# Optimization experiments

Measured on AMD Instinct MI355X. Metric: run time of the kernel, lower is better.

Reference implementation:

```python
import jax, jax.numpy as jnp
import numpy as np

B, L, D, H = 256, 200, 256, 16
Dh = D // H  # value_dim = 16


def setup_inputs() -> dict:
    key = jax.random.key(0)
    ks = jax.random.split(key, 11)
    s = 0.02
    return {
        "news_repr": jax.random.normal(ks[0], (B, L, D), jnp.float32),
        "his_mask": jax.random.randint(ks[1], (B, L, 1), 0, 2, jnp.int32),
        "Wq": jax.random.normal(ks[2], (D, D), jnp.float32) * s,
        "bq": jnp.zeros((D,), jnp.float32),
        "Wk": jax.random.normal(ks[3], (D, D), jnp.float32) * s,
        "bk": jnp.zeros((D,), jnp.float32),
        "Wv": jax.random.normal(ks[4], (D, D), jnp.float32) * s,
        "bv": jnp.zeros((D,), jnp.float32),
        "Wo": jax.random.normal(ks[5], (D, D), jnp.float32) * s,
        "bo": jnp.zeros((D,), jnp.float32),
        "query_news": jax.random.normal(ks[6], (1, D), jnp.float32),
    }


def reference(news_repr, his_mask, Wq, bq, Wk, bk, Wv, bv, Wo, bo, query_news):
    mask = his_mask[..., 0]                                   # [B, L] int
    # get_attn_mask: additive mask, (1 - m) * -10000, broadcast [B,1,1,L]
    add_mask = (1.0 - mask.astype(jnp.float32)) * -10000.0    # [B, L]

    # hand-rolled multi-head attention over the history
    q = (news_repr @ Wq + bq).reshape(B, L, H, Dh)
    k = (news_repr @ Wk + bk).reshape(B, L, H, Dh)
    v = (news_repr @ Wv + bv).reshape(B, L, H, Dh)
    scores = jnp.einsum('bqhd,bkhd->bhqk', q, k) / np.sqrt(Dh)  # [B,H,L,L]
    scores = scores + add_mask[:, None, None, :]
    attn = jax.nn.softmax(scores, axis=-1)
    ctx = jnp.einsum('bhqk,bkhd->bqhd', attn, v).reshape(B, L, D)
    news_out = ctx @ Wo + bo                                   # [B, L, D]

    # scaled_dp_attention pooling against learned query [1, D]
    ps = jnp.einsum('qd,bld->bql', query_news, news_out) / np.sqrt(D)  # [B,1,L]
    ps = jnp.where(mask[:, None, :] > 0, ps, -1e9)
    pattn = jax.nn.softmax(ps, axis=-1)
    user_repr = jnp.einsum('bql,bld->bqd', pattn, news_out)    # [B,1,D]
    return user_repr
```

## Files before the change

kernel.cpp:

```cpp
#include <hip/hip_runtime.h>

typedef unsigned short u16;
typedef unsigned int u32;
typedef unsigned long long u64;
typedef __attribute__((ext_vector_type(8))) short bfrag;
typedef __attribute__((ext_vector_type(4))) short sfrag;
typedef __attribute__((ext_vector_type(4))) float ffrag;


__device__ __forceinline__ float bf2f(u16 u) {
    union { float f; u32 i; } c; c.i = ((u32)u) << 16; return c.f;
}
__device__ __forceinline__ u16 f2bf(float f) {
    union { float f; u32 i; } c; c.f = f;
    u32 r = c.i + 0x7FFFu + ((c.i >> 16) & 1u);
    return (u16)(r >> 16);
}
__device__ __forceinline__ u32 pack2bf(float lo, float hi) {
    union { float f; u32 i; } a, b; a.f = lo; b.f = hi;
    u32 ra = a.i + 0x7FFFu + ((a.i >> 16) & 1u);
    u32 rb = b.i + 0x7FFFu + ((b.i >> 16) & 1u);
    return (ra >> 16) | (rb & 0xFFFF0000u);
}
__device__ __forceinline__ ffrag mfma16(bfrag a, bfrag b, ffrag c) {
    return __builtin_amdgcn_mfma_f32_16x16x32_bf16(a, b, c, 0, 0, 0);
}
__device__ __forceinline__ ffrag mfma16k16(sfrag a, sfrag b, ffrag c) {
    return __builtin_amdgcn_mfma_f32_16x16x16bf16_1k(a, b, c, 0, 0, 0);
}

__global__ __launch_bounds__(256) void wtrans_k(
    const float* __restrict__ W0, const float* __restrict__ W1,
    const float* __restrict__ W2, const float* __restrict__ W3,
    u16* __restrict__ Wt)
{
    __shared__ u16 t_s[64][72];
    const int mat = blockIdx.z;
    const float* W = (mat == 0) ? W0 : (mat == 1) ? W1 : (mat == 2) ? W2 : W3;
    const int k0 = blockIdx.x * 64, n0 = blockIdx.y * 64;
    const int r = threadIdx.x >> 2, cq = threadIdx.x & 3;

    const float* src = W + (size_t)(k0 + r) * 256 + n0 + cq * 16;
#pragma unroll
    for (int j = 0; j < 16; j += 4) {
        float4 f = *(const float4*)(src + j);
        t_s[cq * 16 + j + 0][r] = f2bf(f.x);
        t_s[cq * 16 + j + 1][r] = f2bf(f.y);
        t_s[cq * 16 + j + 2][r] = f2bf(f.z);
        t_s[cq * 16 + j + 3][r] = f2bf(f.w);
    }
    __syncthreads();
    u16* dst = Wt + ((size_t)mat * 256 + n0 + r) * 256 + k0 + cq * 16;
    *(bfrag*)(dst)     = *(const bfrag*)&t_s[r][cq * 16];
    *(bfrag*)(dst + 8) = *(const bfrag*)&t_s[r][cq * 16 + 8];
}

template<bool QKV>
__global__ __launch_bounds__(512) void gemm_k(
    const void* __restrict__ Avp, const u16* __restrict__ Wtp,
    const int* __restrict__ msk,
    const float* __restrict__ b0, const float* __restrict__ b1,
    const float* __restrict__ b2,
    u16* __restrict__ o0, u16* __restrict__ o1, u16* __restrict__ o2)
{
    const int b     = blockIdx.x;
    const int matid = blockIdx.y;
    const int tid = threadIdx.x;
    const int wave = tid >> 6, lane = tid & 63;
    const int quad = lane >> 4, l16 = lane & 15;
    const int wm = wave >> 1, wn = wave & 1;

    __shared__ __align__(16) u16 a_s[4][128][8];
    __shared__ __align__(16) u16 b_s[4][256][8];
    __shared__ u16 idx_s[200];
    __shared__ int wcnt_s[8];

    int m = 0;
    if (tid < 200) m = (msk[b * 200 + tid] != 0) ? 1 : 0;
    u64 bal = __ballot(m);
    if (lane == 0) wcnt_s[wave] = __popcll(bal);
    __syncthreads();
    int cnt = 0;
#pragma unroll
    for (int w = 0; w < 8; w++) cnt += wcnt_s[w];
    if constexpr (QKV) {
        if (cnt == 0) {
            if (tid < 200) idx_s[tid] = (u16)tid;
        } else if (m) {
            int woff = 0;
            for (int w = 0; w < wave; w++) woff += wcnt_s[w];
            idx_s[woff + __popcll(bal & ((1ull << lane) - 1ull))] = (u16)tid;
        }
        __syncthreads();
    }
    if (cnt == 0) cnt = 200;

    const float* Af = (const float*)Avp;
    const u16*   Ab = (const u16*)Avp;

    const int sr = tid >> 2;
    const int sc = tid & 3;
    const u16* Wp = Wtp + (size_t)(matid * 256 + sr) * 256 + sc * 8;

    for (int s0 = 0; s0 < cnt; s0 += 128) {
        const float* apq = nullptr;
        const u16*   apj = nullptr;
        if constexpr (QKV) {
            int i0 = s0 + sr; if (i0 > cnt - 1) i0 = cnt - 1;
            apq = Af + ((size_t)b * 200 + idx_s[i0]) * 256 + sc * 8;
        } else {
            int sl = s0 + sr; if (sl > cnt - 1) sl = cnt - 1;
            apj = Ab + (size_t)b * 51200 + sl * 16;
        }

        ffrag zf = {0.f, 0.f, 0.f, 0.f};
        ffrag acc[2][8];
#pragma unroll
        for (int mi = 0; mi < 2; mi++)
#pragma unroll
            for (int ni = 0; ni < 8; ni++) acc[mi][ni] = zf;

        for (int kk = 0; kk < 256; kk += 32) {
            __syncthreads();
            if constexpr (QKV) {
                float4 f0 = *(const float4*)(apq + kk);
                float4 f1 = *(const float4*)(apq + kk + 4);
                uint4 va = { pack2bf(f0.x, f0.y), pack2bf(f0.z, f0.w),
                             pack2bf(f1.x, f1.y), pack2bf(f1.z, f1.w) };
                *(uint4*)&a_s[sc][sr ^ (sc << 2)][0] = va;
            } else {
                int c = kk + sc * 8;
                size_t hofs = (size_t)(c >> 4) * 3200 + (c & 8);
                *(bfrag*)&a_s[sc][sr ^ (sc << 2)][0] = *(const bfrag*)(apj + hofs);
            }
#pragma unroll
            for (int j = 0; j < 2; j++) {
                int n = sr + j * 128;
                *(bfrag*)&b_s[sc][n ^ (sc << 2)][0] =
                    *(const bfrag*)(Wp + (size_t)j * 128 * 256 + kk);
            }
            __syncthreads();

            bfrag af[2];
#pragma unroll
            for (int mi = 0; mi < 2; mi++) {
                int mm = wm * 32 + mi * 16 + l16;
                af[mi] = *(const bfrag*)&a_s[quad][mm ^ (quad << 2)][0];
            }
#pragma unroll
            for (int ni = 0; ni < 8; ni++) {
                int n = wn * 128 + ni * 16 + l16;
                bfrag bv = *(const bfrag*)&b_s[quad][n ^ (quad << 2)][0];
#pragma unroll
                for (int mi = 0; mi < 2; mi++)
                    acc[mi][ni] = mfma16(af[mi], bv, acc[mi][ni]);
            }
        }

        if constexpr (QKV) {
            const float* bias = (matid == 0) ? b0 : (matid == 1) ? b1 : b2;
            u16* dst = (matid == 0) ? o0 : (matid == 1) ? o1 : o2;
#pragma unroll
            for (int ni = 0; ni < 8; ni++) {
                int nloc = wn * 128 + ni * 16 + l16;
                float bb = bias[nloc];
                size_t hbase = (size_t)b * 51200 + (size_t)(nloc >> 4) * 3200 + (nloc & 15);
#pragma unroll
                for (int mi = 0; mi < 2; mi++) {
                    int slotb = s0 + wm * 32 + mi * 16 + quad * 4;
#pragma unroll
                    for (int r = 0; r < 4; r++) {
                        int slot = slotb + r;
                        if (slot < cnt)
                            dst[hbase + (size_t)slot * 16] = f2bf(acc[mi][ni][r] + bb);
                    }
                }
            }
        } else {
#pragma unroll
            for (int ni = 0; ni < 8; ni++) {
                int col = wn * 128 + ni * 16 + l16;
                float bb = b0[col];
#pragma unroll
                for (int mi = 0; mi < 2; mi++) {
                    int slotb = s0 + wm * 32 + mi * 16 + quad * 4;
#pragma unroll
                    for (int r = 0; r < 4; r++) {
                        int slot = slotb + r;
                        if (slot < cnt)
                            o0[(size_t)b * 51200 + (size_t)slot * 256 + col] = f2bf(acc[mi][ni][r] + bb);
                    }
                }
            }
        }
    }
}

__global__ __launch_bounds__(256) void attn_k(
    u16* __restrict__ Q, const u16* __restrict__ K,
    const u16* __restrict__ V, const int* __restrict__ msk)
{
    const int blk = blockIdx.x;
    const int b = blk >> 4;
    const int tid = threadIdx.x;
    const int wave = tid >> 6, lane = tid & 63;
    const int quad = lane >> 4, l16 = lane & 15;
    const size_t sbase = (size_t)blk * 3200;

    const float SL2E = 0.36067376022224085f;

    __shared__ __align__(8)  u16 kc_s[208][20];
    __shared__ __align__(16) u16 vt_s[16][228];
    __shared__ __align__(16) float am_s[224];
    __shared__ int wcnt_s[4];

    int m = 0;
    if (tid < 200) m = (msk[b * 200 + tid] != 0) ? 1 : 0;
    u64 bal = __ballot(m);
    if (lane == 0) wcnt_s[wave] = __popcll(bal);
    if (tid < 208) {
        u64* z = (u64*)&kc_s[tid][0];
        z[0] = 0; z[1] = 0; z[2] = 0; z[3] = 0;
    }
    u32* vz = (u32*)&vt_s[0][0];
    for (int i = tid; i < 1824; i += 256) vz[i] = 0;
    __syncthreads();

    int cnt = wcnt_s[0] + wcnt_s[1] + wcnt_s[2] + wcnt_s[3];
    if (cnt == 0) cnt = 200;
    for (int i = tid; i < 224; i += 256)
        am_s[i] = (i < cnt) ? 0.f : -1e30f;
    __syncthreads();

    if (tid < cnt) {
        const u64* ks = (const u64*)(K + sbase + tid * 16);
        u64* kd = (u64*)&kc_s[tid][0];
        kd[0] = ks[0]; kd[1] = ks[1]; kd[2] = ks[2]; kd[3] = ks[3];
        const u16* vp = V + sbase + tid * 16;
        bfrag v0 = *(const bfrag*)vp;
        bfrag v1 = *(const bfrag*)(vp + 8);
#pragma unroll
        for (int j = 0; j < 8; j++) {
            vt_s[j][tid]     = (u16)v0[j];
            vt_s[8 + j][tid] = (u16)v1[j];
        }
    }
    __syncthreads();

    const int nt = (cnt + 15) >> 4;

    for (int t = wave; t < nt; t += 4) {
        int lq = t * 16 + l16; if (lq >= cnt) lq = cnt - 1;
        sfrag qf = *(const sfrag*)(Q + sbase + lq * 16 + quad * 4);

        float s[13][4];
#pragma unroll
        for (int kt = 0; kt < 13; kt++) {
            if (kt < nt) {
                sfrag kf = *(const sfrag*)&kc_s[kt * 16 + l16][quad * 4];
                ffrag c = {0.f, 0.f, 0.f, 0.f};
                c = mfma16k16(kf, qf, c);
                ffrag am4 = *(const ffrag*)&am_s[kt * 16 + quad * 4];
#pragma unroll
                for (int r = 0; r < 4; r++)
                    s[kt][r] = __builtin_fmaf(c[r], SL2E, am4[r]);
            }
        }
        float mx = -3e38f;
#pragma unroll
        for (int kt = 0; kt < 13; kt++)
            if (kt < nt)
#pragma unroll
                for (int r = 0; r < 4; r++) mx = fmaxf(mx, s[kt][r]);
        mx = fmaxf(mx, __shfl_xor(mx, 16, 64));
        mx = fmaxf(mx, __shfl_xor(mx, 32, 64));
        float sm = 0.f;
#pragma unroll
        for (int kt = 0; kt < 13; kt++) {
            if (kt < nt) {
                float p0 = __builtin_amdgcn_exp2f(s[kt][0] - mx);
                float p1 = __builtin_amdgcn_exp2f(s[kt][1] - mx);
                float p2 = __builtin_amdgcn_exp2f(s[kt][2] - mx);
                float p3 = __builtin_amdgcn_exp2f(s[kt][3] - mx);
                sm += (p0 + p1) + (p2 + p3);
                s[kt][0] = p0; s[kt][1] = p1; s[kt][2] = p2; s[kt][3] = p3;
            }
        }
        sm += __shfl_xor(sm, 16, 64);
        sm += __shfl_xor(sm, 32, 64);
        float rs = 1.0f / sm;
        ffrag o = {0.f, 0.f, 0.f, 0.f};
#pragma unroll
        for (int kt = 0; kt < 13; kt++) {
            if (kt < nt) {
                union { sfrag v; u32 u[2]; } pk;
                pk.u[0] = pack2bf(s[kt][0] * rs, s[kt][1] * rs);
                pk.u[1] = pack2bf(s[kt][2] * rs, s[kt][3] * rs);
                sfrag bv = *(const sfrag*)&vt_s[l16][kt * 16 + quad * 4];
                o = mfma16k16(pk.v, bv, o);
            }
        }
        int lb = t * 16 + quad * 4;
        u16* qo = Q + sbase + lb * 16 + l16;
#pragma unroll
        for (int r = 0; r < 4; r++) {
            if (lb + r < cnt)
                qo[r * 16] = f2bf(o[r]);
        }
    }
}

__global__ __launch_bounds__(512) void pool_k(
    const u16* __restrict__ NO, const int* __restrict__ msk,
    const float* __restrict__ qn, float* __restrict__ out)
{
    const int b = blockIdx.x;
    const int tid = threadIdx.x;
    const int wave = tid >> 6, lane = tid & 63;

    __shared__ float q_sh[256];
    __shared__ float s_sh[200];
    __shared__ float p_sh[200];
    __shared__ float red_s[16];
    __shared__ float part_s[8][256];
    __shared__ int wcnt_s[4];

    int m = 0;
    if (tid < 200) m = (msk[b * 200 + tid] != 0) ? 1 : 0;
    u64 bal = __ballot(m);
    if (lane == 0 && wave < 4) wcnt_s[wave] = __popcll(bal);
    if (tid < 256) q_sh[tid] = qn[tid];
    __syncthreads();
    int cnt = wcnt_s[0] + wcnt_s[1] + wcnt_s[2] + wcnt_s[3];
    const bool allm = (cnt == 0);
    if (allm) cnt = 200;

    const u16* base = NO + (size_t)b * 51200;

    for (int l = wave; l < cnt; l += 8) {
        u64 v = *(const u64*)(base + l * 256 + lane * 4);
        float d = bf2f((u16)v)         * q_sh[lane * 4 + 0]
                + bf2f((u16)(v >> 16)) * q_sh[lane * 4 + 1]
                + bf2f((u16)(v >> 32)) * q_sh[lane * 4 + 2]
                + bf2f((u16)(v >> 48)) * q_sh[lane * 4 + 3];
#pragma unroll
        for (int dd = 1; dd < 64; dd <<= 1) d += __shfl_xor(d, dd, 64);
        if (lane == 0) s_sh[l] = d * 0.0625f;
    }
    __syncthreads();

    float s = -1e30f;
    if (tid < cnt) s = allm ? -1e9f : s_sh[tid];
    float mw = s;
#pragma unroll
    for (int dd = 1; dd < 64; dd <<= 1) mw = fmaxf(mw, __shfl_xor(mw, dd, 64));
    if (lane == 0) red_s[wave] = mw;
    __syncthreads();
    float mmax = red_s[0];
#pragma unroll
    for (int w = 1; w < 8; w++) mmax = fmaxf(mmax, red_s[w]);
    float e = (tid < cnt) ? __expf(s - mmax) : 0.f;
    float sw = e;
#pragma unroll
    for (int dd = 1; dd < 64; dd <<= 1) sw += __shfl_xor(sw, dd, 64);
    if (lane == 0) red_s[8 + wave] = sw;
    __syncthreads();
    float ssum = 0.f;
#pragma unroll
    for (int w = 0; w < 8; w++) ssum += red_s[8 + w];
    if (tid < cnt) p_sh[tid] = e / ssum;
    __syncthreads();

    float a0 = 0.f, a1 = 0.f, a2 = 0.f, a3 = 0.f;
    for (int l = wave; l < cnt; l += 8) {
        float p = p_sh[l];
        u64 v = *(const u64*)(base + l * 256 + lane * 4);
        a0 += p * bf2f((u16)v);
        a1 += p * bf2f((u16)(v >> 16));
        a2 += p * bf2f((u16)(v >> 32));
        a3 += p * bf2f((u16)(v >> 48));
    }
    part_s[wave][lane * 4 + 0] = a0;
    part_s[wave][lane * 4 + 1] = a1;
    part_s[wave][lane * 4 + 2] = a2;
    part_s[wave][lane * 4 + 3] = a3;
    __syncthreads();
    if (tid < 256) {
        float t = 0.f;
#pragma unroll
        for (int w = 0; w < 8; w++) t += part_s[w][tid];
        out[(size_t)b * 256 + tid] = t;
    }
}

extern "C" void kernel_launch(void* const* d_in, const int* in_sizes, int n_in,
                              void* d_out, int out_size, void* d_ws, size_t ws_size,
                              hipStream_t stream) {
    const float* X   = (const float*)d_in[0];
    const int*   msk = (const int*)d_in[1];
    const float* Wq  = (const float*)d_in[2];
    const float* bq  = (const float*)d_in[3];
    const float* Wk  = (const float*)d_in[4];
    const float* bk  = (const float*)d_in[5];
    const float* Wv  = (const float*)d_in[6];
    const float* bv  = (const float*)d_in[7];
    const float* Wo  = (const float*)d_in[8];
    const float* bo  = (const float*)d_in[9];
    const float* qn  = (const float*)d_in[10];
    float* out = (float*)d_out;

    char* ws = (char*)d_ws;
    u16* qbuf = (u16*)(ws);
    u16* kbuf = (u16*)(ws + 26214400);
    u16* vbuf = (u16*)(ws + 52428800);
    u16* wt   = (u16*)(ws + 78643200);

    wtrans_k<<<dim3(4, 4, 4), 256, 0, stream>>>(Wq, Wk, Wv, Wo, wt);

    gemm_k<true><<<dim3(256, 3), 512, 0, stream>>>(
        X, wt, msk, bq, bk, bv, qbuf, kbuf, vbuf);

    attn_k<<<4096, 256, 0, stream>>>(qbuf, kbuf, vbuf, msk);

    gemm_k<false><<<dim3(256, 1), 512, 0, stream>>>(
        qbuf, wt + 196608, msk, bo, nullptr, nullptr, kbuf, nullptr, nullptr);

    pool_k<<<256, 512, 0, stream>>>(kbuf, msk, qn, out);
}
```

Measured before the change: 187.8 us.

## Fuse output projection GEMM with attention pooling, keeping news_out in LDS

The separate output-projection GEMM and pooling kernels become one kernel, one block per batch. Each block computes ctx@Wo+bo for its valid rows into a ~100KB LDS buffer, then runs the pooled softmax and weighted sum directly from LDS. This removes a kernel launch and the global write and re-read of the bf16 news_out tensor. The cost is a very large LDS footprint, which limits occupancy to about one block per CU, plus scattered 2-byte LDS stores in the epilogue. The QKV GEMM loses its template parameter since only the QKV path remains.

```diff
diff --git a/kernel.cpp b/kernel.cpp
--- a/kernel.cpp
+++ b/kernel.cpp
@@ -55,7 +55,6 @@
     *(bfrag*)(dst + 8) = *(const bfrag*)&t_s[r][cq * 16 + 8];
 }
 
-template<bool QKV>
 __global__ __launch_bounds__(512) void gemm_k(
     const void* __restrict__ Avp, const u16* __restrict__ Wtp,
     const int* __restrict__ msk,
@@ -83,35 +82,25 @@
     int cnt = 0;
 #pragma unroll
     for (int w = 0; w < 8; w++) cnt += wcnt_s[w];
-    if constexpr (QKV) {
-        if (cnt == 0) {
-            if (tid < 200) idx_s[tid] = (u16)tid;
-        } else if (m) {
-            int woff = 0;
-            for (int w = 0; w < wave; w++) woff += wcnt_s[w];
-            idx_s[woff + __popcll(bal & ((1ull << lane) - 1ull))] = (u16)tid;
-        }
-        __syncthreads();
-    }
+    if (cnt == 0) {
+        if (tid < 200) idx_s[tid] = (u16)tid;
+    } else if (m) {
+        int woff = 0;
+        for (int w = 0; w < wave; w++) woff += wcnt_s[w];
+        idx_s[woff + __popcll(bal & ((1ull << lane) - 1ull))] = (u16)tid;
+    }
+    __syncthreads();
     if (cnt == 0) cnt = 200;
 
     const float* Af = (const float*)Avp;
-    const u16*   Ab = (const u16*)Avp;
 
     const int sr = tid >> 2;
     const int sc = tid & 3;
     const u16* Wp = Wtp + (size_t)(matid * 256 + sr) * 256 + sc * 8;
 
     for (int s0 = 0; s0 < cnt; s0 += 128) {
-        const float* apq = nullptr;
-        const u16*   apj = nullptr;
-        if constexpr (QKV) {
-            int i0 = s0 + sr; if (i0 > cnt - 1) i0 = cnt - 1;
-            apq = Af + ((size_t)b * 200 + idx_s[i0]) * 256 + sc * 8;
-        } else {
-            int sl = s0 + sr; if (sl > cnt - 1) sl = cnt - 1;
-            apj = Ab + (size_t)b * 51200 + sl * 16;
-        }
+        int i0 = s0 + sr; if (i0 > cnt - 1) i0 = cnt - 1;
+        const float* apq = Af + ((size_t)b * 200 + idx_s[i0]) * 256 + sc * 8;
 
         ffrag zf = {0.f, 0.f, 0.f, 0.f};
         ffrag acc[2][8];
@@ -122,16 +111,12 @@
 
         for (int kk = 0; kk < 256; kk += 32) {
             __syncthreads();
-            if constexpr (QKV) {
+            {
                 float4 f0 = *(const float4*)(apq + kk);
                 float4 f1 = *(const float4*)(apq + kk + 4);
                 uint4 va = { pack2bf(f0.x, f0.y), pack2bf(f0.z, f0.w),
                              pack2bf(f1.x, f1.y), pack2bf(f1.z, f1.w) };
                 *(uint4*)&a_s[sc][sr ^ (sc << 2)][0] = va;
-            } else {
-                int c = kk + sc * 8;
-                size_t hofs = (size_t)(c >> 4) * 3200 + (c & 8);
-                *(bfrag*)&a_s[sc][sr ^ (sc << 2)][0] = *(const bfrag*)(apj + hofs);
             }
 #pragma unroll
             for (int j = 0; j < 2; j++) {
@@ -157,39 +142,21 @@
             }
         }
 
-        if constexpr (QKV) {
-            const float* bias = (matid == 0) ? b0 : (matid == 1) ? b1 : b2;
-            u16* dst = (matid == 0) ? o0 : (matid == 1) ? o1 : o2;
-#pragma unroll
-            for (int ni = 0; ni < 8; ni++) {
-                int nloc = wn * 128 + ni * 16 + l16;
-                float bb = bias[nloc];
-                size_t hbase = (size_t)b * 51200 + (size_t)(nloc >> 4) * 3200 + (nloc & 15);
-#pragma unroll
-                for (int mi = 0; mi < 2; mi++) {
-                    int slotb = s0 + wm * 32 + mi * 16 + quad * 4;
-#pragma unroll
-                    for (int r = 0; r < 4; r++) {
-                        int slot = slotb + r;
-                        if (slot < cnt)
-                            dst[hbase + (size_t)slot * 16] = f2bf(acc[mi][ni][r] + bb);
-                    }
-                }
-            }
-        } else {
-#pragma unroll
-            for (int ni = 0; ni < 8; ni++) {
-                int col = wn * 128 + ni * 16 + l16;
-                float bb = b0[col];
-#pragma unroll
-                for (int mi = 0; mi < 2; mi++) {
-                    int slotb = s0 + wm * 32 + mi * 16 + quad * 4;
-#pragma unroll
-                    for (int r = 0; r < 4; r++) {
-                        int slot = slotb + r;
-                        if (slot < cnt)
-                            o0[(size_t)b * 51200 + (size_t)slot * 256 + col] = f2bf(acc[mi][ni][r] + bb);
-                    }
+        const float* bias = (matid == 0) ? b0 : (matid == 1) ? b1 : b2;
+        u16* dst = (matid == 0) ? o0 : (matid == 1) ? o1 : o2;
+#pragma unroll
+        for (int ni = 0; ni < 8; ni++) {
+            int nloc = wn * 128 + ni * 16 + l16;
+            float bb = bias[nloc];
+            size_t hbase = (size_t)b * 51200 + (size_t)(nloc >> 4) * 3200 + (nloc & 15);
+#pragma unroll
+            for (int mi = 0; mi < 2; mi++) {
+                int slotb = s0 + wm * 32 + mi * 16 + quad * 4;
+#pragma unroll
+                for (int r = 0; r < 4; r++) {
+                    int slot = slotb + r;
+                    if (slot < cnt)
+                        dst[hbase + (size_t)slot * 16] = f2bf(acc[mi][ni][r] + bb);
                 }
             }
         }
@@ -310,35 +277,108 @@
     }
 }
 
-__global__ __launch_bounds__(512) void pool_k(
-    const u16* __restrict__ NO, const int* __restrict__ msk,
-    const float* __restrict__ qn, float* __restrict__ out)
+__global__ __launch_bounds__(512) void projpool_k(
+    const u16* __restrict__ ctx,
+    const u16* __restrict__ Wt,
+    const float* __restrict__ bo,
+    const int* __restrict__ msk,
+    const float* __restrict__ qn,
+    float* __restrict__ out)
 {
     const int b = blockIdx.x;
     const int tid = threadIdx.x;
     const int wave = tid >> 6, lane = tid & 63;
-
+    const int quad = lane >> 4, l16 = lane & 15;
+    const int wm = wave >> 1, wn = wave & 1;
+
+    __shared__ __align__(16) u16 no_s[200][256];
+    __shared__ __align__(16) u16 a_s[4][128][8];
+    __shared__ __align__(16) u16 b_s[4][256][8];
     __shared__ float q_sh[256];
     __shared__ float s_sh[200];
     __shared__ float p_sh[200];
     __shared__ float red_s[16];
     __shared__ float part_s[8][256];
-    __shared__ int wcnt_s[4];
+    __shared__ int wcnt_s[8];
 
     int m = 0;
     if (tid < 200) m = (msk[b * 200 + tid] != 0) ? 1 : 0;
     u64 bal = __ballot(m);
-    if (lane == 0 && wave < 4) wcnt_s[wave] = __popcll(bal);
+    if (lane == 0) wcnt_s[wave] = __popcll(bal);
     if (tid < 256) q_sh[tid] = qn[tid];
     __syncthreads();
-    int cnt = wcnt_s[0] + wcnt_s[1] + wcnt_s[2] + wcnt_s[3];
+    int cnt = 0;
+#pragma unroll
+    for (int w = 0; w < 8; w++) cnt += wcnt_s[w];
     const bool allm = (cnt == 0);
     if (allm) cnt = 200;
 
-    const u16* base = NO + (size_t)b * 51200;
+    const int sr = tid >> 2;
+    const int sc = tid & 3;
+    const u16* Wp = Wt + (size_t)sr * 256 + sc * 8;
+
+    for (int s0 = 0; s0 < cnt; s0 += 128) {
+        int sl = s0 + sr; if (sl > cnt - 1) sl = cnt - 1;
+        const u16* apj = ctx + (size_t)b * 51200 + sl * 16;
+
+        ffrag zf = {0.f, 0.f, 0.f, 0.f};
+        ffrag acc[2][8];
+#pragma unroll
+        for (int mi = 0; mi < 2; mi++)
+#pragma unroll
+            for (int ni = 0; ni < 8; ni++) acc[mi][ni] = zf;
+
+        for (int kk = 0; kk < 256; kk += 32) {
+            __syncthreads();
+            {
+                int c = kk + sc * 8;
+                size_t hofs = (size_t)(c >> 4) * 3200 + (c & 8);
+                *(bfrag*)&a_s[sc][sr ^ (sc << 2)][0] = *(const bfrag*)(apj + hofs);
+            }
+#pragma unroll
+            for (int j = 0; j < 2; j++) {
+                int n = sr + j * 128;
+                *(bfrag*)&b_s[sc][n ^ (sc << 2)][0] =
+                    *(const bfrag*)(Wp + (size_t)j * 128 * 256 + kk);
+            }
+            __syncthreads();
+
+            bfrag af[2];
+#pragma unroll
+            for (int mi = 0; mi < 2; mi++) {
+                int mm = wm * 32 + mi * 16 + l16;
+                af[mi] = *(const bfrag*)&a_s[quad][mm ^ (quad << 2)][0];
+            }
+#pragma unroll
+            for (int ni = 0; ni < 8; ni++) {
+                int n = wn * 128 + ni * 16 + l16;
+                bfrag bv = *(const bfrag*)&b_s[quad][n ^ (quad << 2)][0];
+#pragma unroll
+                for (int mi = 0; mi < 2; mi++)
+                    acc[mi][ni] = mfma16(af[mi], bv, acc[mi][ni]);
+            }
+        }
+
+#pragma unroll
+        for (int ni = 0; ni < 8; ni++) {
+            int col = wn * 128 + ni * 16 + l16;
+            float bb = bo[col];
+#pragma unroll
+            for (int mi = 0; mi < 2; mi++) {
+                int slotb = s0 + wm * 32 + mi * 16 + quad * 4;
+#pragma unroll
+                for (int r = 0; r < 4; r++) {
+                    int slot = slotb + r;
+                    if (slot < cnt)
+                        no_s[slot][col] = f2bf(acc[mi][ni][r] + bb);
+                }
+            }
+        }
+    }
+    __syncthreads();
 
     for (int l = wave; l < cnt; l += 8) {
-        u64 v = *(const u64*)(base + l * 256 + lane * 4);
+        u64 v = *(const u64*)&no_s[l][lane * 4];
         float d = bf2f((u16)v)         * q_sh[lane * 4 + 0]
                 + bf2f((u16)(v >> 16)) * q_sh[lane * 4 + 1]
                 + bf2f((u16)(v >> 32)) * q_sh[lane * 4 + 2]
@@ -374,7 +414,7 @@
     float a0 = 0.f, a1 = 0.f, a2 = 0.f, a3 = 0.f;
     for (int l = wave; l < cnt; l += 8) {
         float p = p_sh[l];
-        u64 v = *(const u64*)(base + l * 256 + lane * 4);
+        u64 v = *(const u64*)&no_s[l][lane * 4];
         a0 += p * bf2f((u16)v);
         a1 += p * bf2f((u16)(v >> 16));
         a2 += p * bf2f((u16)(v >> 32));
@@ -417,13 +457,11 @@
 
     wtrans_k<<<dim3(4, 4, 4), 256, 0, stream>>>(Wq, Wk, Wv, Wo, wt);
 
-    gemm_k<true><<<dim3(256, 3), 512, 0, stream>>>(
+    gemm_k<<<dim3(256, 3), 512, 0, stream>>>(
         X, wt, msk, bq, bk, bv, qbuf, kbuf, vbuf);
 
     attn_k<<<4096, 256, 0, stream>>>(qbuf, kbuf, vbuf, msk);
 
-    gemm_k<false><<<dim3(256, 1), 512, 0, stream>>>(
-        qbuf, wt + 196608, msk, bo, nullptr, nullptr, kbuf, nullptr, nullptr);
-
-    pool_k<<<256, 512, 0, stream>>>(kbuf, msk, qn, out);
-}
+    projpool_k<<<256, 512, 0, stream>>>(
+        qbuf, wt + 196608, bo, msk, qn, out);
+}
```

New measurement: 180.7 us. -3.8%, faster.

## Fold output projection into pooling via linearity, dropping the Wo GEMM

Applied to the files above, without the earlier changes.

The output projection Wo is moved past the attention pooling using linearity. Pooling scores become ctx·(Wo·q), and the pooled context is projected by Wo once per batch. This removes the full per-token Wo GEMM kernel, its weight transpose and the bf16 write and reread of news_out. Each pool block now stages its ctx tile (about 100 KB) in shared memory and does two 256x256 matrix-vector products, which lowers occupancy and is less parallel.

```diff
diff --git a/kernel.cpp b/kernel.cpp
--- a/kernel.cpp
+++ b/kernel.cpp
@@ -31,12 +31,12 @@
 
 __global__ __launch_bounds__(256) void wtrans_k(
     const float* __restrict__ W0, const float* __restrict__ W1,
-    const float* __restrict__ W2, const float* __restrict__ W3,
+    const float* __restrict__ W2,
     u16* __restrict__ Wt)
 {
     __shared__ u16 t_s[64][72];
     const int mat = blockIdx.z;
-    const float* W = (mat == 0) ? W0 : (mat == 1) ? W1 : (mat == 2) ? W2 : W3;
+    const float* W = (mat == 0) ? W0 : (mat == 1) ? W1 : W2;
     const int k0 = blockIdx.x * 64, n0 = blockIdx.y * 64;
     const int r = threadIdx.x >> 2, cq = threadIdx.x & 3;
 
@@ -55,7 +55,6 @@
     *(bfrag*)(dst + 8) = *(const bfrag*)&t_s[r][cq * 16 + 8];
 }
 
-template<bool QKV>
 __global__ __launch_bounds__(512) void gemm_k(
     const void* __restrict__ Avp, const u16* __restrict__ Wtp,
     const int* __restrict__ msk,
@@ -83,35 +82,25 @@
     int cnt = 0;
 #pragma unroll
     for (int w = 0; w < 8; w++) cnt += wcnt_s[w];
-    if constexpr (QKV) {
-        if (cnt == 0) {
-            if (tid < 200) idx_s[tid] = (u16)tid;
-        } else if (m) {
-            int woff = 0;
-            for (int w = 0; w < wave; w++) woff += wcnt_s[w];
-            idx_s[woff + __popcll(bal & ((1ull << lane) - 1ull))] = (u16)tid;
-        }
-        __syncthreads();
-    }
+    if (cnt == 0) {
+        if (tid < 200) idx_s[tid] = (u16)tid;
+    } else if (m) {
+        int woff = 0;
+        for (int w = 0; w < wave; w++) woff += wcnt_s[w];
+        idx_s[woff + __popcll(bal & ((1ull << lane) - 1ull))] = (u16)tid;
+    }
+    __syncthreads();
     if (cnt == 0) cnt = 200;
 
     const float* Af = (const float*)Avp;
-    const u16*   Ab = (const u16*)Avp;
 
     const int sr = tid >> 2;
     const int sc = tid & 3;
     const u16* Wp = Wtp + (size_t)(matid * 256 + sr) * 256 + sc * 8;
 
     for (int s0 = 0; s0 < cnt; s0 += 128) {
-        const float* apq = nullptr;
-        const u16*   apj = nullptr;
-        if constexpr (QKV) {
-            int i0 = s0 + sr; if (i0 > cnt - 1) i0 = cnt - 1;
-            apq = Af + ((size_t)b * 200 + idx_s[i0]) * 256 + sc * 8;
-        } else {
-            int sl = s0 + sr; if (sl > cnt - 1) sl = cnt - 1;
-            apj = Ab + (size_t)b * 51200 + sl * 16;
-        }
+        int i0 = s0 + sr; if (i0 > cnt - 1) i0 = cnt - 1;
+        const float* apq = Af + ((size_t)b * 200 + idx_s[i0]) * 256 + sc * 8;
 
         ffrag zf = {0.f, 0.f, 0.f, 0.f};
         ffrag acc[2][8];
@@ -122,16 +111,12 @@
 
         for (int kk = 0; kk < 256; kk += 32) {
             __syncthreads();
-            if constexpr (QKV) {
+            {
                 float4 f0 = *(const float4*)(apq + kk);
                 float4 f1 = *(const float4*)(apq + kk + 4);
                 uint4 va = { pack2bf(f0.x, f0.y), pack2bf(f0.z, f0.w),
                              pack2bf(f1.x, f1.y), pack2bf(f1.z, f1.w) };
                 *(uint4*)&a_s[sc][sr ^ (sc << 2)][0] = va;
-            } else {
-                int c = kk + sc * 8;
-                size_t hofs = (size_t)(c >> 4) * 3200 + (c & 8);
-                *(bfrag*)&a_s[sc][sr ^ (sc << 2)][0] = *(const bfrag*)(apj + hofs);
             }
 #pragma unroll
             for (int j = 0; j < 2; j++) {
@@ -157,39 +142,21 @@
             }
         }
 
-        if constexpr (QKV) {
-            const float* bias = (matid == 0) ? b0 : (matid == 1) ? b1 : b2;
-            u16* dst = (matid == 0) ? o0 : (matid == 1) ? o1 : o2;
-#pragma unroll
-            for (int ni = 0; ni < 8; ni++) {
-                int nloc = wn * 128 + ni * 16 + l16;
-                float bb = bias[nloc];
-                size_t hbase = (size_t)b * 51200 + (size_t)(nloc >> 4) * 3200 + (nloc & 15);
-#pragma unroll
-                for (int mi = 0; mi < 2; mi++) {
-                    int slotb = s0 + wm * 32 + mi * 16 + quad * 4;
-#pragma unroll
-                    for (int r = 0; r < 4; r++) {
-                        int slot = slotb + r;
-                        if (slot < cnt)
-                            dst[hbase + (size_t)slot * 16] = f2bf(acc[mi][ni][r] + bb);
-                    }
-                }
-            }
-        } else {
-#pragma unroll
-            for (int ni = 0; ni < 8; ni++) {
-                int col = wn * 128 + ni * 16 + l16;
-                float bb = b0[col];
-#pragma unroll
-                for (int mi = 0; mi < 2; mi++) {
-                    int slotb = s0 + wm * 32 + mi * 16 + quad * 4;
-#pragma unroll
-                    for (int r = 0; r < 4; r++) {
-                        int slot = slotb + r;
-                        if (slot < cnt)
-                            o0[(size_t)b * 51200 + (size_t)slot * 256 + col] = f2bf(acc[mi][ni][r] + bb);
-                    }
+        const float* bias = (matid == 0) ? b0 : (matid == 1) ? b1 : b2;
+        u16* dst = (matid == 0) ? o0 : (matid == 1) ? o1 : o2;
+#pragma unroll
+        for (int ni = 0; ni < 8; ni++) {
+            int nloc = wn * 128 + ni * 16 + l16;
+            float bb = bias[nloc];
+            size_t hbase = (size_t)b * 51200 + (size_t)(nloc >> 4) * 3200 + (nloc & 15);
+#pragma unroll
+            for (int mi = 0; mi < 2; mi++) {
+                int slotb = s0 + wm * 32 + mi * 16 + quad * 4;
+#pragma unroll
+                for (int r = 0; r < 4; r++) {
+                    int slot = slotb + r;
+                    if (slot < cnt)
+                        dst[hbase + (size_t)slot * 16] = f2bf(acc[mi][ni][r] + bb);
                 }
             }
         }
@@ -310,39 +277,66 @@
     }
 }
 
-__global__ __launch_bounds__(512) void pool_k(
-    const u16* __restrict__ NO, const int* __restrict__ msk,
-    const float* __restrict__ qn, float* __restrict__ out)
+__global__ __launch_bounds__(512) void pool_k2(
+    const u16* __restrict__ ctx,
+    const float* __restrict__ Wo,
+    const float* __restrict__ bo,
+    const int* __restrict__ msk,
+    const float* __restrict__ qn,
+    float* __restrict__ out)
 {
     const int b = blockIdx.x;
     const int tid = threadIdx.x;
     const int wave = tid >> 6, lane = tid & 63;
 
+    __shared__ __align__(16) u16 ctx_s[200][256];
     __shared__ float q_sh[256];
+    __shared__ float wt_sh[256];
     __shared__ float s_sh[200];
     __shared__ float p_sh[200];
     __shared__ float red_s[16];
     __shared__ float part_s[8][256];
-    __shared__ int wcnt_s[4];
+    __shared__ int wcnt_s[8];
 
     int m = 0;
     if (tid < 200) m = (msk[b * 200 + tid] != 0) ? 1 : 0;
     u64 bal = __ballot(m);
-    if (lane == 0 && wave < 4) wcnt_s[wave] = __popcll(bal);
+    if (lane == 0) wcnt_s[wave] = __popcll(bal);
     if (tid < 256) q_sh[tid] = qn[tid];
     __syncthreads();
-    int cnt = wcnt_s[0] + wcnt_s[1] + wcnt_s[2] + wcnt_s[3];
+    int cnt = 0;
+#pragma unroll
+    for (int w = 0; w < 8; w++) cnt += wcnt_s[w];
     const bool allm = (cnt == 0);
     if (allm) cnt = 200;
 
-    const u16* base = NO + (size_t)b * 51200;
+    const u16* cb = ctx + (size_t)b * 51200;
+    for (int i = tid; i < 3200; i += 512) {
+        int h = i / 200, l = i - h * 200;
+        if (l < cnt) {
+            const bfrag* src = (const bfrag*)(cb + h * 3200 + l * 16);
+            *(bfrag*)&ctx_s[l][h * 16]     = src[0];
+            *(bfrag*)&ctx_s[l][h * 16 + 8] = src[1];
+        }
+    }
+    if (tid < 256) {
+        const float* wr = Wo + (size_t)tid * 256;
+        float a = 0.f;
+        for (int d = 0; d < 256; d += 4) {
+            float4 wv = *(const float4*)(wr + d);
+            a += wv.x * q_sh[d] + wv.y * q_sh[d + 1]
+               + wv.z * q_sh[d + 2] + wv.w * q_sh[d + 3];
+        }
+        wt_sh[tid] = a;
+    }
+    __syncthreads();
 
     for (int l = wave; l < cnt; l += 8) {
-        u64 v = *(const u64*)(base + l * 256 + lane * 4);
-        float d = bf2f((u16)v)         * q_sh[lane * 4 + 0]
-                + bf2f((u16)(v >> 16)) * q_sh[lane * 4 + 1]
-                + bf2f((u16)(v >> 32)) * q_sh[lane * 4 + 2]
-                + bf2f((u16)(v >> 48)) * q_sh[lane * 4 + 3];
+        u64 v = *(const u64*)&ctx_s[l][lane * 4];
+        float d = bf2f((u16)v)         * wt_sh[lane * 4 + 0]
+                + bf2f((u16)(v >> 16)) * wt_sh[lane * 4 + 1]
+                + bf2f((u16)(v >> 32)) * wt_sh[lane * 4 + 2]
+                + bf2f((u16)(v >> 48)) * wt_sh[lane * 4 + 3];
 #pragma unroll
         for (int dd = 1; dd < 64; dd <<= 1) d += __shfl_xor(d, dd, 64);
         if (lane == 0) s_sh[l] = d * 0.0625f;
@@ -374,7 +368,7 @@
     float a0 = 0.f, a1 = 0.f, a2 = 0.f, a3 = 0.f;
     for (int l = wave; l < cnt; l += 8) {
         float p = p_sh[l];
-        u64 v = *(const u64*)(base + l * 256 + lane * 4);
+        u64 v = *(const u64*)&ctx_s[l][lane * 4];
         a0 += p * bf2f((u16)v);
         a1 += p * bf2f((u16)(v >> 16));
         a2 += p * bf2f((u16)(v >> 32));
@@ -389,7 +383,16 @@
         float t = 0.f;
 #pragma unroll
         for (int w = 0; w < 8; w++) t += part_s[w][tid];
-        out[(size_t)b * 256 + tid] = t;
+        wt_sh[tid] = t;
+    }
+    __syncthreads();
+
+    if (tid < 256) {
+        float o = bo[tid];
+        const float* wc = Wo + tid;
+        for (int k = 0; k < 256; k++)
+            o = __builtin_fmaf(wt_sh[k], wc[(size_t)k * 256], o);
+        out[(size_t)b * 256 + tid] = o;
     }
 }
 
@@ -415,15 +418,13 @@
     u16* vbuf = (u16*)(ws + 52428800);
     u16* wt   = (u16*)(ws + 78643200);
 
-    wtrans_k<<<dim3(4, 4, 4), 256, 0, stream>>>(Wq, Wk, Wv, Wo, wt);
-
-    gemm_k<true><<<dim3(256, 3), 512, 0, stream>>>(
+    wtrans_k<<<dim3(4, 4, 3), 256, 0, stream>>>(Wq, Wk, Wv, wt);
+
+    gemm_k<<<dim3(256, 3), 512, 0, stream>>>(
         X, wt, msk, bq, bk, bv, qbuf, kbuf, vbuf);
 
     attn_k<<<4096, 256, 0, stream>>>(qbuf, kbuf, vbuf, msk);
 
-    gemm_k<false><<<dim3(256, 1), 512, 0, stream>>>(
-        qbuf, wt + 196608, msk, bo, nullptr, nullptr, kbuf, nullptr, nullptr);
-
-    pool_k<<<256, 512, 0, stream>>>(kbuf, msk, qn, out);
-}
+    pool_k2<<<256, 512, 0, stream>>>(
+        qbuf, Wo, bo, msk, qn, out);
+}
```

After: 184.3 us. About the same (-1.9%).
